# Kernel optimization log

Hardware: AMD Instinct MI355X
Metric: run time of the kernel (lower is better)

## Reference

```python
import jax, jax.numpy as jnp
import numpy as np

N_NODES = 60000
N_EDGES = 300000
FACE_DIM = 32
EDGE_DIM = 16
GF = 64   # EGAT node/edge hidden dim
EF = 32   # NNConv output dim
FF = 32   # placeholder point-transformer dim (zeros path)
TOT = GF + EF + FF  # 128
NEG_SLOPE = 0.01    # torch LeakyReLU default inside DGL EGATConv


def _leaky(x):
    return jnp.where(x >= 0, x, NEG_SLOPE * x)


def _edge_softmax(logits, dst, n):
    # softmax over incoming edges of each destination node (DGL edge_softmax)
    m = jax.ops.segment_max(logits, dst, num_segments=n)
    e = jnp.exp(logits - m[dst])
    s = jax.ops.segment_sum(e, dst, num_segments=n)
    return e / s[dst]


def _egat(h, f, src, dst, n, w_ni, w_nj, w_fij, w_node, attn, bias):
    # DGL EGATConv with num_heads=1 (head dim squeezed)
    f_out = _leaky((h @ w_ni)[src] + (h @ w_nj)[dst] + f @ w_fij + bias)  # (E, GF)
    a = _edge_softmax(f_out @ attn, dst, n)                               # (E,)
    msg = (h @ w_node)[src] * a[:, None]                                  # (E, GF)
    h_out = jax.ops.segment_sum(msg, dst, num_segments=n)                 # (N, GF)
    return h_out, f_out


def setup_inputs() -> dict:
    key = jax.random.key(0)
    ks = iter(jax.random.split(key, 40))

    def w(shape, scale=0.1):
        return jax.random.normal(next(ks), shape, dtype=jnp.float32) * scale

    inp = {
        "face_features": jax.random.normal(next(ks), (N_NODES, FACE_DIM), dtype=jnp.float32),
        "edge_features": jax.random.normal(next(ks), (N_EDGES, EDGE_DIM), dtype=jnp.float32),
        "fp_w": w((FACE_DIM, GF)), "fp_b": w((GF,)),
        "ep_w": w((EDGE_DIM, GF)), "ep_b": w((GF,)),
        "nn_w": w((EDGE_DIM, FACE_DIM * EF), 0.05), "nn_b": w((FACE_DIM * EF,), 0.05),
        "nn_bias": w((EF,)),
        "gate_w": w((TOT, 1)), "gate_b": w((1,)),
        "src": jax.random.randint(next(ks), (N_EDGES,), 0, N_NODES),
        "dst": jax.random.randint(next(ks), (N_EDGES,), 0, N_NODES),
    }
    for L in ("e1", "e2"):
        inp[f"{L}_ni"] = w((GF, GF))
        inp[f"{L}_nj"] = w((GF, GF))
        inp[f"{L}_fij"] = w((GF, GF))
        inp[f"{L}_node"] = w((GF, GF))
        inp[f"{L}_attn"] = w((GF,))
        inp[f"{L}_bias"] = w((GF,))
    return inp


def reference(face_features, edge_features, fp_w, fp_b, ep_w, ep_b,
              nn_w, nn_b, nn_bias, gate_w, gate_b,
              e1_ni, e1_nj, e1_fij, e1_node, e1_attn, e1_bias,
              e2_ni, e2_nj, e2_fij, e2_node, e2_attn, e2_bias,
              src, dst):
    n = face_features.shape[0]
    # --- Gf: two stacked EGATConv layers on projected features ---
    h = face_features @ fp_w + fp_b
    f = edge_features @ ep_w + ep_b
    h, f = _egat(h, f, src, dst, n, e1_ni, e1_nj, e1_fij, e1_node, e1_attn, e1_bias)
    h, f = _egat(h, f, src, dst, n, e2_ni, e2_nj, e2_fij, e2_node, e2_attn, e2_bias)
    Gf = h
    # --- Ef: NNConv (edge-conditioned conv, mean aggregation) ---
    W_e = (edge_features @ nn_w + nn_b).reshape(-1, FACE_DIM, EF)      # (E, 32, 32)
    m = jnp.einsum('ei,eio->eo', face_features[src], W_e)              # (E, EF)
    s = jax.ops.segment_sum(m, dst, num_segments=n)
    cnt = jax.ops.segment_sum(jnp.ones((m.shape[0],), m.dtype), dst, num_segments=n)
    Ef_feat = s / jnp.maximum(cnt, 1.0)[:, None] + nn_bias             # (N, EF)
    # --- Ff: zeros (face_point_features=None path) ---
    Ff_feat = jnp.zeros((n, FF), dtype=Gf.dtype)
    node_features = jnp.concatenate([Gf, Ef_feat, Ff_feat], axis=-1)   # (N, 128)
    # --- GlobalAttentionPooling (single graph) ---
    gate = jax.nn.softmax(node_features @ gate_w + gate_b, axis=0)     # (N, 1)
    graph_feat = jnp.sum(gate * node_features, axis=0, keepdims=True)  # (1, 128)
    return node_features, graph_feat
```

## Files before the change

kernel.cpp:

```cpp
#include <hip/hip_runtime.h>

#define NN 60000
#define NE 300000
#define PB 768
typedef unsigned short ush;
typedef __attribute__((ext_vector_type(8))) short bf16x8;
typedef __attribute__((ext_vector_type(4))) float f32x4;

static inline int cdiv(int a, int b) { return (a + b - 1) / b; }

__device__ inline unsigned ord_enc(float x) {
  unsigned u = __float_as_uint(x);
  return (u & 0x80000000u) ? ~u : (u | 0x80000000u);
}
__device__ inline float ord_dec(unsigned u) {
  return __uint_as_float((u & 0x80000000u) ? (u & 0x7fffffffu) : ~u);
}
__device__ inline float bf2f(unsigned u16) { return __uint_as_float(u16 << 16); }
__device__ inline ush f2bf(float x) {
  unsigned u = __float_as_uint(x);
  return (ush)((u + 0x7FFFu + ((u >> 16) & 1u)) >> 16);
}
__device__ inline unsigned pack2(float lo, float hi) {
  return ((unsigned)f2bf(hi) << 16) | (unsigned)f2bf(lo);
}

__global__ void deg_kernel(const int* __restrict__ key, int* __restrict__ deg) {
  int e = blockIdx.x * blockDim.x + threadIdx.x;
  if (e < NE) atomicAdd(deg + key[e], 1);
}

__global__ void scan1_kernel(const int* __restrict__ deg, int* __restrict__ rowptr,
                             int* __restrict__ partial) {
  __shared__ int s[256];
  int i = blockIdx.x * 256 + threadIdx.x;
  int v = (i < NN) ? deg[i] : 0;
  s[threadIdx.x] = v;
  __syncthreads();
  for (int off = 1; off < 256; off <<= 1) {
    int t = (threadIdx.x >= off) ? s[threadIdx.x - off] : 0;
    __syncthreads();
    s[threadIdx.x] += t;
    __syncthreads();
  }
  if (i < NN) rowptr[i] = s[threadIdx.x] - v;
  if (threadIdx.x == 255) partial[blockIdx.x] = s[255];
}

__global__ void scan2_kernel(int* __restrict__ partial, int nb) {
  __shared__ int s[256];
  int v = (threadIdx.x < nb) ? partial[threadIdx.x] : 0;
  s[threadIdx.x] = v;
  __syncthreads();
  for (int off = 1; off < 256; off <<= 1) {
    int t = (threadIdx.x >= off) ? s[threadIdx.x - off] : 0;
    __syncthreads();
    s[threadIdx.x] += t;
    __syncthreads();
  }
  if (threadIdx.x < nb) partial[threadIdx.x] = s[threadIdx.x] - v;
}

__global__ void scan3_kernel(int* __restrict__ rowptr, const int* __restrict__ partial,
                             int* __restrict__ cursor) {
  int i = blockIdx.x * 256 + threadIdx.x;
  if (i < NN) {
    int r = rowptr[i] + partial[blockIdx.x];
    rowptr[i] = r;
    cursor[i] = r;
  }
}

__global__ void scatter_dst_kernel(const int* __restrict__ src, const int* __restrict__ dst,
                                   const float* __restrict__ ef, int* __restrict__ cursor,
                                   int* __restrict__ src_s, int* __restrict__ dst_s,
                                   float* __restrict__ ef_s) {
  int e = blockIdx.x * blockDim.x + threadIdx.x;
  if (e >= NE) return;
  int d = dst[e];
  int j = atomicAdd(cursor + d, 1);
  src_s[j] = src[e];
  dst_s[j] = d;
  const float4* ep = (const float4*)(ef + (size_t)e * 16);
  float4 a = ep[0], b = ep[1], c = ep[2], dd = ep[3];
  float4* op = (float4*)(ef_s + (size_t)j * 16);
  op[0] = a; op[1] = b; op[2] = c; op[3] = dd;
}

__global__ void fold_kernel(const float* __restrict__ fp_w, const float* __restrict__ fp_b,
                            const float* __restrict__ ep_w, const float* __restrict__ ep_b,
                            const float* __restrict__ fij, const float* __restrict__ ebias,
                            const float* __restrict__ ni, const float* __restrict__ nj,
                            const float* __restrict__ node, float* __restrict__ fold) {
  int t = blockIdx.x * blockDim.x + threadIdx.x;
  if (t >= 7424) return;
  int o = t & 63;
  const float* A;
  const float* B;
  float init = 0.f;
  if (t < 1024)      { A = ep_w + (size_t)(t >> 6) * 64; B = fij + o; }
  else if (t < 1088) { A = ep_b; B = fij + o; init = ebias[o]; }
  else if (t < 3136) { A = fp_w + (size_t)((t - 1088) >> 6) * 64; B = ni + o; }
  else if (t < 5184) { A = fp_w + (size_t)((t - 3136) >> 6) * 64; B = nj + o; }
  else if (t < 7232) { A = fp_w + (size_t)((t - 5184) >> 6) * 64; B = node + o; }
  else if (t < 7296) { A = fp_b; B = ni + o; }
  else if (t < 7360) { A = fp_b; B = nj + o; }
  else               { A = fp_b; B = node + o; }
  float a = init;
  for (int i = 0; i < 64; ++i) a = fmaf(A[i], B[(size_t)i * 64], a);
  fold[t] = a;
}

__global__ void nnwt_frag_kernel(const float* __restrict__ nn_w, const float* __restrict__ nn_b,
                                 ush* __restrict__ Wfrag) {
  int t = blockIdx.x * blockDim.x + threadIdx.x;
  if (t >= 17408) return;
  int i = t & 7, lane = (t >> 3) & 63, ct = (t >> 9) & 1, kk = t >> 10;
  int k = kk * 32 + (lane >> 4) * 8 + i;
  int o = ct * 16 + (lane & 15);
  float v = (k < 512) ? nn_w[(size_t)(k >> 5) * 1024 + (k & 31) * 32 + o]
                      : nn_b[(k - 512) * 32 + o];
  Wfrag[t] = f2bf(v);
}

__global__ void fij_frag_kernel(const float* __restrict__ fij, ush* __restrict__ Wfrag2) {
  int t = blockIdx.x * blockDim.x + threadIdx.x;
  if (t >= 4096) return;
  int i = t & 7, lane = (t >> 3) & 63, ct = (t >> 9) & 3, kk = t >> 11;
  int k = kk * 32 + (lane >> 4) * 8 + i;
  int o = ct * 16 + (lane & 15);
  Wfrag2[t] = f2bf(fij[(size_t)k * 64 + o]);
}

__global__ void hproj_frag_kernel(const float* __restrict__ ni, const float* __restrict__ nj,
                                  const float* __restrict__ node, ush* __restrict__ WfragH) {
  int t = blockIdx.x * blockDim.x + threadIdx.x;
  if (t >= 12288) return;
  int i = t & 7, lane = (t >> 3) & 63, ct = (t >> 9) & 3, kk = (t >> 11) & 1, m = t >> 12;
  int k = kk * 32 + (lane >> 4) * 8 + i;
  int o = ct * 16 + (lane & 15);
  const float* W = (m == 0) ? ni : (m == 1) ? nj : node;
  WfragH[t] = f2bf(W[(size_t)k * 64 + o]);
}

template <int K, bool BIAS>
__global__ __launch_bounds__(256, 2) void gemm3_kernel(
    const float* __restrict__ A, const float* __restrict__ W0, const float* __restrict__ W1,
    const float* __restrict__ W2, const float* __restrict__ b0, const float* __restrict__ b1,
    const float* __restrict__ b2, ush* __restrict__ o0, ush* __restrict__ o1,
    ush* __restrict__ o2, int rows) {
  __shared__ float sA[128][K + 1];
  __shared__ float sW[K][64];
  const float* W = blockIdx.y == 0 ? W0 : blockIdx.y == 1 ? W1 : W2;
  const float* bb = blockIdx.y == 0 ? b0 : blockIdx.y == 1 ? b1 : b2;
  ush* out = blockIdx.y == 0 ? o0 : blockIdx.y == 1 ? o1 : o2;
  int t = threadIdx.x;
  int r0 = blockIdx.x * 128;
  for (int i = t; i < K * 16; i += 256) ((float4*)sW)[i] = ((const float4*)W)[i];
  for (int i = t; i < 128 * (K / 4); i += 256) {
    int rr = i / (K / 4), cc = i % (K / 4);
    float4 v = (r0 + rr < rows) ? ((const float4*)(A + (size_t)(r0 + rr) * K))[cc]
                                : make_float4(0.f, 0.f, 0.f, 0.f);
    sA[rr][cc * 4 + 0] = v.x;
    sA[rr][cc * 4 + 1] = v.y;
    sA[rr][cc * 4 + 2] = v.z;
    sA[rr][cc * 4 + 3] = v.w;
  }
  __syncthreads();
  int rg = t >> 3, cg = t & 7;
  float acc[4][8];
#pragma unroll
  for (int i = 0; i < 4; ++i)
#pragma unroll
    for (int j = 0; j < 8; ++j) acc[i][j] = 0.f;
#pragma unroll 8
  for (int k = 0; k < K; ++k) {
    float a0 = sA[rg * 4 + 0][k], a1 = sA[rg * 4 + 1][k];
    float a2 = sA[rg * 4 + 2][k], a3 = sA[rg * 4 + 3][k];
    float4 wA = *(const float4*)&sW[k][cg * 8];
    float4 wB = *(const float4*)&sW[k][cg * 8 + 4];
#pragma unroll
    for (int i = 0; i < 4; ++i) {
      float a = i == 0 ? a0 : i == 1 ? a1 : i == 2 ? a2 : a3;
      acc[i][0] = fmaf(a, wA.x, acc[i][0]); acc[i][1] = fmaf(a, wA.y, acc[i][1]);
      acc[i][2] = fmaf(a, wA.z, acc[i][2]); acc[i][3] = fmaf(a, wA.w, acc[i][3]);
      acc[i][4] = fmaf(a, wB.x, acc[i][4]); acc[i][5] = fmaf(a, wB.y, acc[i][5]);
      acc[i][6] = fmaf(a, wB.z, acc[i][6]); acc[i][7] = fmaf(a, wB.w, acc[i][7]);
    }
  }
  float bv[8];
#pragma unroll
  for (int j = 0; j < 8; ++j) bv[j] = BIAS ? bb[cg * 8 + j] : 0.f;
#pragma unroll
  for (int i = 0; i < 4; ++i) {
    int r = r0 + rg * 4 + i;
    if (r < rows) {
      uint4 pv;
      pv.x = pack2(acc[i][0] + bv[0], acc[i][1] + bv[1]);
      pv.y = pack2(acc[i][2] + bv[2], acc[i][3] + bv[3]);
      pv.z = pack2(acc[i][4] + bv[4], acc[i][5] + bv[5]);
      pv.w = pack2(acc[i][6] + bv[6], acc[i][7] + bv[7]);
      *(uint4*)(out + (size_t)r * 64 + cg * 8) = pv;
    }
  }
}

template <int K, bool STORE>
__global__ __launch_bounds__(256, 2) void gemm_fout_kernel(
    const float* __restrict__ A, const float* __restrict__ W, const float* __restrict__ bias,
    const ush* __restrict__ hs, const ush* __restrict__ hd, const int* __restrict__ src_s,
    const int* __restrict__ dst_s, const float* __restrict__ attn, ush* __restrict__ fstore,
    float* __restrict__ logit) {
  __shared__ float sA[128][K + 1];
  __shared__ float sW[K][64];
  int t = threadIdx.x;
  int r0 = blockIdx.x * 128;
  for (int i = t; i < K * 16; i += 256) ((float4*)sW)[i] = ((const float4*)W)[i];
  for (int i = t; i < 128 * (K / 4); i += 256) {
    int rr = i / (K / 4), cc = i % (K / 4);
    float4 v = (r0 + rr < NE) ? ((const float4*)(A + (size_t)(r0 + rr) * K))[cc]
                              : make_float4(0.f, 0.f, 0.f, 0.f);
    sA[rr][cc * 4 + 0] = v.x;
    sA[rr][cc * 4 + 1] = v.y;
    sA[rr][cc * 4 + 2] = v.z;
    sA[rr][cc * 4 + 3] = v.w;
  }
  __syncthreads();
  int rg = t >> 3, cg = t & 7;
  float acc[4][8];
#pragma unroll
  for (int i = 0; i < 4; ++i)
#pragma unroll
    for (int j = 0; j < 8; ++j) acc[i][j] = 0.f;
#pragma unroll 8
  for (int k = 0; k < K; ++k) {
    float a0 = sA[rg * 4 + 0][k], a1 = sA[rg * 4 + 1][k];
    float a2 = sA[rg * 4 + 2][k], a3 = sA[rg * 4 + 3][k];
    float4 wA = *(const float4*)&sW[k][cg * 8];
    float4 wB = *(const float4*)&sW[k][cg * 8 + 4];
#pragma unroll
    for (int i = 0; i < 4; ++i) {
      float a = i == 0 ? a0 : i == 1 ? a1 : i == 2 ? a2 : a3;
      acc[i][0] = fmaf(a, wA.x, acc[i][0]); acc[i][1] = fmaf(a, wA.y, acc[i][1]);
      acc[i][2] = fmaf(a, wA.z, acc[i][2]); acc[i][3] = fmaf(a, wA.w, acc[i][3]);
      acc[i][4] = fmaf(a, wB.x, acc[i][4]); acc[i][5] = fmaf(a, wB.y, acc[i][5]);
      acc[i][6] = fmaf(a, wB.z, acc[i][6]); acc[i][7] = fmaf(a, wB.w, acc[i][7]);
    }
  }
  float bv[8], av[8];
#pragma unroll
  for (int j = 0; j < 8; ++j) {
    bv[j] = bias[cg * 8 + j];
    av[j] = attn[cg * 8 + j];
  }
#pragma unroll
  for (int i = 0; i < 4; ++i) {
    int r = r0 + rg * 4 + i;
    if (r < NE) {
      int s = src_s[r], d = dst_s[r];
      uint4 hv = *(const uint4*)(hs + (size_t)s * 64 + cg * 8);
      uint4 dv = *(const uint4*)(hd + (size_t)d * 64 + cg * 8);
      float fo[8];
      fo[0] = acc[i][0] + bf2f(hv.x & 0xffff) + bf2f(dv.x & 0xffff) + bv[0];
      fo[1] = acc[i][1] + bf2f(hv.x >> 16)    + bf2f(dv.x >> 16)    + bv[1];
      fo[2] = acc[i][2] + bf2f(hv.y & 0xffff) + bf2f(dv.y & 0xffff) + bv[2];
      fo[3] = acc[i][3] + bf2f(hv.y >> 16)    + bf2f(dv.y >> 16)    + bv[3];
      fo[4] = acc[i][4] + bf2f(hv.z & 0xffff) + bf2f(dv.z & 0xffff) + bv[4];
      fo[5] = acc[i][5] + bf2f(hv.z >> 16)    + bf2f(dv.z >> 16)    + bv[5];
      fo[6] = acc[i][6] + bf2f(hv.w & 0xffff) + bf2f(dv.w & 0xffff) + bv[6];
      fo[7] = acc[i][7] + bf2f(hv.w >> 16)    + bf2f(dv.w >> 16)    + bv[7];
      float p = 0.f;
#pragma unroll
      for (int j = 0; j < 8; ++j) {
        fo[j] = fo[j] >= 0.f ? fo[j] : 0.01f * fo[j];
        p = fmaf(fo[j], av[j], p);
      }
      if (STORE) {
        uint4 pv;
        pv.x = pack2(fo[0], fo[1]);
        pv.y = pack2(fo[2], fo[3]);
        pv.z = pack2(fo[4], fo[5]);
        pv.w = pack2(fo[6], fo[7]);
        *(uint4*)(fstore + (size_t)r * 64 + cg * 8) = pv;
      }
      p += __shfl_xor(p, 1, 64);
      p += __shfl_xor(p, 2, 64);
      p += __shfl_xor(p, 4, 64);
      if (cg == 0) logit[r] = p;
    }
  }
}

__global__ __launch_bounds__(256, 4) void mfma_hproj_kernel(
    const ush* __restrict__ h1bf, const ush* __restrict__ WfragH, ush* __restrict__ hs,
    ush* __restrict__ hd, ush* __restrict__ hn) {
  int wave = (blockIdx.x * blockDim.x + threadIdx.x) >> 6;
  int lane = threadIdx.x & 63;
  int m0 = wave * 16;
  if (m0 >= NN) return;
  int arow = lane & 15;
  int aoff = (lane >> 4) * 8;
  const ush* ap = h1bf + (size_t)(m0 + arow) * 64 + aoff;
  bf16x8 a0 = *(const bf16x8*)(ap);
  bf16x8 a1 = *(const bf16x8*)(ap + 32);
  const ush* wp = WfragH + lane * 8;
  int ccol = lane & 15;
  int crow = (lane >> 4) * 4;
#pragma unroll
  for (int m = 0; m < 3; ++m) {
    f32x4 acc0 = {0.f, 0.f, 0.f, 0.f};
    f32x4 acc1 = {0.f, 0.f, 0.f, 0.f};
    f32x4 acc2 = {0.f, 0.f, 0.f, 0.f};
    f32x4 acc3 = {0.f, 0.f, 0.f, 0.f};
    const ush* wm = wp + (size_t)m * 8 * 512;
    bf16x8 b0 = *(const bf16x8*)(wm + 0 * 512);
    bf16x8 b1 = *(const bf16x8*)(wm + 1 * 512);
    bf16x8 b2 = *(const bf16x8*)(wm + 2 * 512);
    bf16x8 b3 = *(const bf16x8*)(wm + 3 * 512);
    acc0 = __builtin_amdgcn_mfma_f32_16x16x32_bf16(a0, b0, acc0, 0, 0, 0);
    acc1 = __builtin_amdgcn_mfma_f32_16x16x32_bf16(a0, b1, acc1, 0, 0, 0);
    acc2 = __builtin_amdgcn_mfma_f32_16x16x32_bf16(a0, b2, acc2, 0, 0, 0);
    acc3 = __builtin_amdgcn_mfma_f32_16x16x32_bf16(a0, b3, acc3, 0, 0, 0);
    b0 = *(const bf16x8*)(wm + 4 * 512);
    b1 = *(const bf16x8*)(wm + 5 * 512);
    b2 = *(const bf16x8*)(wm + 6 * 512);
    b3 = *(const bf16x8*)(wm + 7 * 512);
    acc0 = __builtin_amdgcn_mfma_f32_16x16x32_bf16(a1, b0, acc0, 0, 0, 0);
    acc1 = __builtin_amdgcn_mfma_f32_16x16x32_bf16(a1, b1, acc1, 0, 0, 0);
    acc2 = __builtin_amdgcn_mfma_f32_16x16x32_bf16(a1, b2, acc2, 0, 0, 0);
    acc3 = __builtin_amdgcn_mfma_f32_16x16x32_bf16(a1, b3, acc3, 0, 0, 0);
    ush* outm = (m == 0) ? hs : (m == 1) ? hd : hn;
#pragma unroll
    for (int j = 0; j < 4; ++j) {
      ush* op = outm + (size_t)(m0 + crow + j) * 64;
      op[ccol] = f2bf(acc0[j]);
      op[16 + ccol] = f2bf(acc1[j]);
      op[32 + ccol] = f2bf(acc2[j]);
      op[48 + ccol] = f2bf(acc3[j]);
    }
  }
}

__global__ __launch_bounds__(256, 4) void mfma_fout_kernel(
    const ush* __restrict__ f116, const ush* __restrict__ Wfrag2, const float* __restrict__ bias,
    const ush* __restrict__ hs, const ush* __restrict__ hd, const int* __restrict__ src_s,
    const int* __restrict__ dst_s, const float* __restrict__ attn, float* __restrict__ logit) {
  int wave = (blockIdx.x * blockDim.x + threadIdx.x) >> 6;
  int lane = threadIdx.x & 63;
  int m0 = wave * 16;
  if (m0 >= NE) return;
  int arow = lane & 15;
  int aoff = (lane >> 4) * 8;
  const ush* ap = f116 + (size_t)(m0 + arow) * 64 + aoff;
  const ush* wp = Wfrag2 + lane * 8;
  f32x4 acc0 = {0.f, 0.f, 0.f, 0.f};
  f32x4 acc1 = {0.f, 0.f, 0.f, 0.f};
  f32x4 acc2 = {0.f, 0.f, 0.f, 0.f};
  f32x4 acc3 = {0.f, 0.f, 0.f, 0.f};
#pragma unroll
  for (int kk = 0; kk < 2; ++kk) {
    bf16x8 a = *(const bf16x8*)(ap + kk * 32);
    bf16x8 b0 = *(const bf16x8*)(wp + (size_t)(kk * 4 + 0) * 512);
    bf16x8 b1 = *(const bf16x8*)(wp + (size_t)(kk * 4 + 1) * 512);
    bf16x8 b2 = *(const bf16x8*)(wp + (size_t)(kk * 4 + 2) * 512);
    bf16x8 b3 = *(const bf16x8*)(wp + (size_t)(kk * 4 + 3) * 512);
    acc0 = __builtin_amdgcn_mfma_f32_16x16x32_bf16(a, b0, acc0, 0, 0, 0);
    acc1 = __builtin_amdgcn_mfma_f32_16x16x32_bf16(a, b1, acc1, 0, 0, 0);
    acc2 = __builtin_amdgcn_mfma_f32_16x16x32_bf16(a, b2, acc2, 0, 0, 0);
    acc3 = __builtin_amdgcn_mfma_f32_16x16x32_bf16(a, b3, acc3, 0, 0, 0);
  }
  int ccol = lane & 15;
  int crow = (lane >> 4) * 4;
  float av0 = attn[ccol], av1 = attn[16 + ccol], av2 = attn[32 + ccol], av3 = attn[48 + ccol];
  float bv0 = bias[ccol], bv1 = bias[16 + ccol], bv2 = bias[32 + ccol], bv3 = bias[48 + ccol];
#pragma unroll
  for (int j = 0; j < 4; ++j) {
    int r = m0 + crow + j;
    int s = src_s[r], d = dst_s[r];
    const ush* hsp = hs + (size_t)s * 64;
    const ush* hdp = hd + (size_t)d * 64;
    float f0 = acc0[j] + bf2f(hsp[ccol]) + bf2f(hdp[ccol]) + bv0;
    float f1 = acc1[j] + bf2f(hsp[16 + ccol]) + bf2f(hdp[16 + ccol]) + bv1;
    float f2 = acc2[j] + bf2f(hsp[32 + ccol]) + bf2f(hdp[32 + ccol]) + bv2;
    float f3 = acc3[j] + bf2f(hsp[48 + ccol]) + bf2f(hdp[48 + ccol]) + bv3;
    f0 = f0 >= 0.f ? f0 : 0.01f * f0;
    f1 = f1 >= 0.f ? f1 : 0.01f * f1;
    f2 = f2 >= 0.f ? f2 : 0.01f * f2;
    f3 = f3 >= 0.f ? f3 : 0.01f * f3;
    float p = fmaf(f0, av0, fmaf(f1, av1, fmaf(f2, av2, f3 * av3)));
    p += __shfl_xor(p, 1, 64);
    p += __shfl_xor(p, 2, 64);
    p += __shfl_xor(p, 4, 64);
    p += __shfl_xor(p, 8, 64);
    if (ccol == 0) logit[r] = p;
  }
}

template <bool BF16OUT>
__global__ __launch_bounds__(256, 4) void agg_gather_kernel(
    const ush* __restrict__ hn, const float* __restrict__ logit, const int* __restrict__ rowptr,
    const int* __restrict__ deg, const int* __restrict__ src_s, void* __restrict__ hnew) {
  int wave = (blockIdx.x * blockDim.x + threadIdx.x) >> 6;
  int lane = threadIdx.x & 63;
  if (wave >= NN) return;
  int n = wave, d = deg[n], r0 = rowptr[n];
  if (d == 0) {
    if (BF16OUT) ((ush*)hnew)[(size_t)n * 64 + lane] = 0;
    else ((float*)hnew)[(size_t)n * 64 + lane] = 0.f;
    return;
  }
  float sum = 0.f, acc0 = 0.f, acc1 = 0.f, acc2 = 0.f, acc3 = 0.f;
  int j = 0;
  for (; j + 3 < d; j += 4) {
    int jj = r0 + j;
    int s0 = src_s[jj + 0], s1 = src_s[jj + 1], s2 = src_s[jj + 2], s3 = src_s[jj + 3];
    float l0 = logit[jj + 0], l1 = logit[jj + 1], l2 = logit[jj + 2], l3 = logit[jj + 3];
    ush h0 = hn[(size_t)s0 * 64 + lane];
    ush h1 = hn[(size_t)s1 * 64 + lane];
    ush h2 = hn[(size_t)s2 * 64 + lane];
    ush h3 = hn[(size_t)s3 * 64 + lane];
    float w0 = __expf(l0), w1 = __expf(l1);
    float w2 = __expf(l2), w3 = __expf(l3);
    sum += (w0 + w1) + (w2 + w3);
    acc0 = fmaf(w0, bf2f(h0), acc0);
    acc1 = fmaf(w1, bf2f(h1), acc1);
    acc2 = fmaf(w2, bf2f(h2), acc2);
    acc3 = fmaf(w3, bf2f(h3), acc3);
  }
  for (; j < d; ++j) {
    int jj = r0 + j;
    float w = __expf(logit[jj]);
    sum += w;
    acc0 = fmaf(w, bf2f(hn[(size_t)src_s[jj] * 64 + lane]), acc0);
  }
  float r = ((acc0 + acc1) + (acc2 + acc3)) / sum;
  if (BF16OUT) ((ush*)hnew)[(size_t)n * 64 + lane] = f2bf(r);
  else ((float*)hnew)[(size_t)n * 64 + lane] = r;
}

__global__ __launch_bounds__(256, 4) void nnconv_G_kernel(
    const float* __restrict__ face, const float* __restrict__ ef_s,
    const int* __restrict__ rowptr, const int* __restrict__ deg, const int* __restrict__ src_s,
    ush* __restrict__ G) {
  int wave = (blockIdx.x * blockDim.x + threadIdx.x) >> 6;
  int lane = threadIdx.x & 63;
  if (wave >= NN) return;
  int n = wave, d = deg[n], r0 = rowptr[n];
  int k4 = lane >> 2, ib = lane & 3;
  float g[8], fs[8];
#pragma unroll
  for (int u = 0; u < 8; ++u) { g[u] = 0.f; fs[u] = 0.f; }
  int j = 0;
  for (; j + 1 < d; j += 2) {
    int jj = r0 + j;
    int s0 = src_s[jj], s1 = src_s[jj + 1];
    float ev0 = ef_s[(size_t)jj * 16 + k4];
    float ev1 = ef_s[(size_t)(jj + 1) * 16 + k4];
    const float4* fp0 = (const float4*)(face + (size_t)s0 * 32 + ib * 8);
    const float4* fp1 = (const float4*)(face + (size_t)s1 * 32 + ib * 8);
    float4 fa0 = fp0[0], fb0 = fp0[1];
    float4 fa1 = fp1[0], fb1 = fp1[1];
    g[0] = fmaf(ev0, fa0.x, g[0]); g[1] = fmaf(ev0, fa0.y, g[1]);
    g[2] = fmaf(ev0, fa0.z, g[2]); g[3] = fmaf(ev0, fa0.w, g[3]);
    g[4] = fmaf(ev0, fb0.x, g[4]); g[5] = fmaf(ev0, fb0.y, g[5]);
    g[6] = fmaf(ev0, fb0.z, g[6]); g[7] = fmaf(ev0, fb0.w, g[7]);
    g[0] = fmaf(ev1, fa1.x, g[0]); g[1] = fmaf(ev1, fa1.y, g[1]);
    g[2] = fmaf(ev1, fa1.z, g[2]); g[3] = fmaf(ev1, fa1.w, g[3]);
    g[4] = fmaf(ev1, fb1.x, g[4]); g[5] = fmaf(ev1, fb1.y, g[5]);
    g[6] = fmaf(ev1, fb1.z, g[6]); g[7] = fmaf(ev1, fb1.w, g[7]);
    if (k4 == 0) {
      fs[0] += fa0.x + fa1.x; fs[1] += fa0.y + fa1.y;
      fs[2] += fa0.z + fa1.z; fs[3] += fa0.w + fa1.w;
      fs[4] += fb0.x + fb1.x; fs[5] += fb0.y + fb1.y;
      fs[6] += fb0.z + fb1.z; fs[7] += fb0.w + fb1.w;
    }
  }
  if (j < d) {
    int jj = r0 + j;
    int s0 = src_s[jj];
    float ev0 = ef_s[(size_t)jj * 16 + k4];
    const float4* fp0 = (const float4*)(face + (size_t)s0 * 32 + ib * 8);
    float4 fa0 = fp0[0], fb0 = fp0[1];
    g[0] = fmaf(ev0, fa0.x, g[0]); g[1] = fmaf(ev0, fa0.y, g[1]);
    g[2] = fmaf(ev0, fa0.z, g[2]); g[3] = fmaf(ev0, fa0.w, g[3]);
    g[4] = fmaf(ev0, fb0.x, g[4]); g[5] = fmaf(ev0, fb0.y, g[5]);
    g[6] = fmaf(ev0, fb0.z, g[6]); g[7] = fmaf(ev0, fb0.w, g[7]);
    if (k4 == 0) {
      fs[0] += fa0.x; fs[1] += fa0.y; fs[2] += fa0.z; fs[3] += fa0.w;
      fs[4] += fb0.x; fs[5] += fb0.y; fs[6] += fb0.z; fs[7] += fb0.w;
    }
  }
  uint4 pv;
  pv.x = pack2(g[0], g[1]); pv.y = pack2(g[2], g[3]);
  pv.z = pack2(g[4], g[5]); pv.w = pack2(g[6], g[7]);
  *(uint4*)(G + (size_t)n * 544 + lane * 8) = pv;
  if (k4 == 0) {
    uint4 fv;
    fv.x = pack2(fs[0], fs[1]); fv.y = pack2(fs[2], fs[3]);
    fv.z = pack2(fs[4], fs[5]); fv.w = pack2(fs[6], fs[7]);
    *(uint4*)(G + (size_t)n * 544 + 512 + ib * 8) = fv;
  }
}

__global__ __launch_bounds__(256, 4) void gemm_G_mfma_kernel(const ush* __restrict__ G,
                                                             const ush* __restrict__ Wfrag,
                                                             float* __restrict__ sArr,
                                                             int rows) {
  int wave = (blockIdx.x * blockDim.x + threadIdx.x) >> 6;
  int lane = threadIdx.x & 63;
  int m0 = wave * 16;
  if (m0 >= rows) return;
  int arow = lane & 15;
  int aoff = (lane >> 4) * 8;
  const ush* gp = G + (size_t)(m0 + arow) * 544 + aoff;
  const ush* wp = Wfrag + lane * 8;
  f32x4 acc0 = {0.f, 0.f, 0.f, 0.f};
  f32x4 acc1 = {0.f, 0.f, 0.f, 0.f};
#pragma unroll 4
  for (int kk = 0; kk < 17; ++kk) {
    bf16x8 a = *(const bf16x8*)(gp + kk * 32);
    bf16x8 b0 = *(const bf16x8*)(wp + (size_t)(kk * 2 + 0) * 512);
    bf16x8 b1 = *(const bf16x8*)(wp + (size_t)(kk * 2 + 1) * 512);
    acc0 = __builtin_amdgcn_mfma_f32_16x16x32_bf16(a, b0, acc0, 0, 0, 0);
    acc1 = __builtin_amdgcn_mfma_f32_16x16x32_bf16(a, b1, acc1, 0, 0, 0);
  }
  int ccol = lane & 15;
  int crow = (lane >> 4) * 4;
#pragma unroll
  for (int j = 0; j < 4; ++j) {
    int r = m0 + crow + j;
    sArr[(size_t)r * 32 + ccol] = acc0[j];
    sArr[(size_t)r * 32 + 16 + ccol] = acc1[j];
  }
}

__global__ void combine_gate_kernel(const float* __restrict__ hfin, const float* __restrict__ sArr,
                                    const int* __restrict__ deg, const float* __restrict__ nn_bias,
                                    const float* __restrict__ gate_w, const float* __restrict__ gate_b,
                                    float* __restrict__ out, float* __restrict__ g) {
  int wave = (blockIdx.x * blockDim.x + threadIdx.x) >> 6;
  int lane = threadIdx.x & 63;
  if (wave >= NN) return;
  int n = wave;
  float v0 = hfin[(size_t)n * 64 + lane];
  int c1 = lane + 64;
  float v1 = (c1 < 96)
                 ? sArr[(size_t)n * 32 + (c1 - 64)] / fmaxf((float)deg[n], 1.0f) + nn_bias[c1 - 64]
                 : 0.f;
  out[(size_t)n * 128 + lane] = v0;
  out[(size_t)n * 128 + c1] = v1;
  float p = v0 * gate_w[lane] + ((c1 < 96) ? v1 * gate_w[c1] : 0.f);
#pragma unroll
  for (int off = 32; off; off >>= 1) p += __shfl_xor(p, off, 64);
  if (lane == 0) g[n] = p + gate_b[0];
}

__global__ void gate_max_kernel(const float* __restrict__ g, unsigned* __restrict__ gmax) {
  int tid = blockIdx.x * blockDim.x + threadIdx.x;
  int stride = gridDim.x * blockDim.x;
  float v = -3.0e38f;
  for (int n = tid; n < NN; n += stride) v = fmaxf(v, g[n]);
#pragma unroll
  for (int off = 32; off; off >>= 1) v = fmaxf(v, __shfl_xor(v, off, 64));
  __shared__ float sm[4];
  int lane = threadIdx.x & 63, wid = threadIdx.x >> 6;
  if (lane == 0) sm[wid] = v;
  __syncthreads();
  if (threadIdx.x == 0) {
    float m = fmaxf(fmaxf(sm[0], sm[1]), fmaxf(sm[2], sm[3]));
    atomicMax(gmax, ord_enc(m));
  }
}

__global__ __launch_bounds__(256, 4) void pool_exp_kernel(
    const float* __restrict__ nf, const float* __restrict__ g, const unsigned* __restrict__ gmax,
    float* __restrict__ pacc, float* __restrict__ wsb) {
  int o = threadIdx.x & 127;
  int half = threadIdx.x >> 7;
  int ri = blockIdx.x * 2 + half;
  float m = ord_dec(*gmax);
  float acc0 = 0.f, acc1 = 0.f, ws = 0.f;
  int n = ri;
  const int STR = PB * 2;
  for (; n + STR < NN; n += STR * 2) {
    float w0 = __expf(g[n] - m);
    float w1 = __expf(g[n + STR] - m);
    float v0 = nf[(size_t)n * 128 + o];
    float v1 = nf[(size_t)(n + STR) * 128 + o];
    ws += w0 + w1;
    acc0 = fmaf(w0, v0, acc0);
    acc1 = fmaf(w1, v1, acc1);
  }
  if (n < NN) {
    float w = __expf(g[n] - m);
    ws += w;
    acc0 = fmaf(w, nf[(size_t)n * 128 + o], acc0);
  }
  pacc[(size_t)ri * 128 + o] = acc0 + acc1;
  if (o == 0) wsb[ri] = ws;
}

__global__ void pool_reduce_kernel(const float* __restrict__ pacc, const float* __restrict__ wsb,
                                   float* __restrict__ gacc, float* __restrict__ gsum) {
  int b = blockIdx.x;
  int t = threadIdx.x;
  float v = 0.f;
  if (b < 128) {
    for (int ri = t; ri < PB * 2; ri += 256) v += pacc[(size_t)ri * 128 + b];
  } else {
    for (int ri = t; ri < PB * 2; ri += 256) v += wsb[ri];
  }
#pragma unroll
  for (int off = 32; off; off >>= 1) v += __shfl_xor(v, off, 64);
  __shared__ float sm[4];
  int lane = t & 63, wid = t >> 6;
  if (lane == 0) sm[wid] = v;
  __syncthreads();
  if (t == 0) {
    float s = (sm[0] + sm[1]) + (sm[2] + sm[3]);
    if (b < 128) gacc[b] = s;
    else gsum[0] = s;
  }
}

__global__ void finalize_kernel(const float* __restrict__ gacc, const float* __restrict__ gsum,
                                float* __restrict__ out) {
  int o = threadIdx.x;
  if (o < 128) out[(size_t)NN * 128 + o] = gacc[o] / gsum[0];
}

extern "C" void kernel_launch(void* const* d_in, const int* in_sizes, int n_in,
                              void* d_out, int out_size, void* d_ws, size_t ws_size,
                              hipStream_t stream) {
  const float* face    = (const float*)d_in[0];
  const float* ef      = (const float*)d_in[1];
  const float* fp_w    = (const float*)d_in[2];
  const float* fp_b    = (const float*)d_in[3];
  const float* ep_w    = (const float*)d_in[4];
  const float* ep_b    = (const float*)d_in[5];
  const float* nn_w    = (const float*)d_in[6];
  const float* nn_b    = (const float*)d_in[7];
  const float* nn_bias = (const float*)d_in[8];
  const float* gate_w  = (const float*)d_in[9];
  const float* gate_b  = (const float*)d_in[10];
  const int*   src     = (const int*)d_in[11];
  const int*   dst     = (const int*)d_in[12];
  const float* e1_attn = (const float*)d_in[17];
  const float* e2_ni   = (const float*)d_in[19];
  const float* e2_nj   = (const float*)d_in[20];
  const float* e2_fij  = (const float*)d_in[21];
  const float* e2_attn = (const float*)d_in[23];
  const float* e2_bias = (const float*)d_in[24];
  float* out = (float*)d_out;

  char* p = (char*)d_ws;
  auto alloc = [&](size_t nfloats) {
    float* r = (float*)p;
    p += ((nfloats * 4 + 255) / 256) * 256;
    return r;
  };
  float* h0 = alloc((size_t)NN * 64);
  ush* h1bf = (ush*)alloc((size_t)NN * 32);
  char* bigreg = p;
  ush* hs16 = (ush*)alloc((size_t)NN * 32);
  ush* hd16 = (ush*)alloc((size_t)NN * 32);
  ush* hn16 = (ush*)alloc((size_t)NN * 32);
  ush* f116 = (ush*)alloc((size_t)NE * 32);
  float* logit = alloc(NE);
  {
    size_t used = (size_t)(p - bigreg);
    size_t need = (size_t)NN * 544 * 2;
    if (used < need) p += ((need - used + 255) / 256) * 256;
  }
  ush* G = (ush*)bigreg;
  float* sArr  = alloc((size_t)NN * 32);
  float* g     = alloc(NN);
  float* gacc  = alloc(128);
  float* gsum  = alloc(1);
  unsigned* gmax = (unsigned*)alloc(1);
  float* fold  = alloc(7424);
  ush* Wfrag   = (ush*)alloc(17408 / 2);
  ush* Wfrag2  = (ush*)alloc(4096 / 2);
  ush* WfragH  = (ush*)alloc(12288 / 2);
  float* pacc  = alloc((size_t)PB * 2 * 128);
  float* wsb   = alloc(PB * 2);
  int* deg    = (int*)alloc(NN);
  int* rowptr = (int*)alloc(NN);
  int* cursor = (int*)alloc(NN);
  int* partial = (int*)alloc(256);
  int* src_s  = (int*)alloc(NE);
  int* dst_s  = (int*)alloc(NE);
  float* ef_s = alloc((size_t)NE * 16);

  const float* Wf1  = fold;
  const float* b1f  = fold + 1024;
  const float* Wni1 = fold + 1088;
  const float* Wnj1 = fold + 3136;
  const float* Wno1 = fold + 5184;
  const float* bni1 = fold + 7232;
  const float* bnj1 = fold + 7296;
  const float* bno1 = fold + 7360;

  const int B = 256;
  const int NGB = cdiv(NN, 128);
  const int EGB = cdiv(NE, 128);
  const int NB256 = cdiv(NN, 256);

  hipMemsetAsync(deg, 0, NN * 4, stream);
  deg_kernel<<<cdiv(NE, B), B, 0, stream>>>(dst, deg);
  scan1_kernel<<<NB256, 256, 0, stream>>>(deg, rowptr, partial);
  scan2_kernel<<<1, 256, 0, stream>>>(partial, NB256);
  scan3_kernel<<<NB256, 256, 0, stream>>>(rowptr, partial, cursor);
  scatter_dst_kernel<<<cdiv(NE, B), B, 0, stream>>>(src, dst, ef, cursor, src_s, dst_s, ef_s);

  fold_kernel<<<29, B, 0, stream>>>(fp_w, fp_b, ep_w, ep_b,
                                    (const float*)d_in[15], (const float*)d_in[18],
                                    (const float*)d_in[13], (const float*)d_in[14],
                                    (const float*)d_in[16], fold);
  nnwt_frag_kernel<<<68, B, 0, stream>>>(nn_w, nn_b, Wfrag);
  fij_frag_kernel<<<16, B, 0, stream>>>(e2_fij, Wfrag2);
  hproj_frag_kernel<<<48, B, 0, stream>>>(e2_ni, e2_nj, (const float*)d_in[22], WfragH);

  gemm3_kernel<32, true><<<dim3(NGB, 3), B, 0, stream>>>(face, Wni1, Wnj1, Wno1, bni1, bnj1,
                                                         bno1, hs16, hd16, hn16, NN);
  gemm_fout_kernel<16, true><<<EGB, B, 0, stream>>>(ef_s, Wf1, b1f, hs16, hd16, src_s,
                                                    dst_s, e1_attn, f116, logit);
  agg_gather_kernel<true><<<cdiv(NN * 64, B), B, 0, stream>>>(hn16, logit, rowptr, deg,
                                                              src_s, h1bf);

  mfma_hproj_kernel<<<cdiv(NN * 4, B), B, 0, stream>>>(h1bf, WfragH, hs16, hd16, hn16);
  mfma_fout_kernel<<<cdiv(NE * 4, B), B, 0, stream>>>(f116, Wfrag2, e2_bias, hs16, hd16,
                                                      src_s, dst_s, e2_attn, logit);
  agg_gather_kernel<false><<<cdiv(NN * 64, B), B, 0, stream>>>(hn16, logit, rowptr, deg,
                                                               src_s, h0);

  nnconv_G_kernel<<<cdiv(NN * 64, B), B, 0, stream>>>(face, ef_s, rowptr, deg, src_s, G);
  gemm_G_mfma_kernel<<<cdiv(NN * 4, B), B, 0, stream>>>(G, Wfrag, sArr, NN);

  hipMemsetAsync(gmax, 0, 4, stream);
  combine_gate_kernel<<<cdiv(NN * 64, B), B, 0, stream>>>(h0, sArr, deg, nn_bias, gate_w,
                                                          gate_b, out, g);
  gate_max_kernel<<<128, B, 0, stream>>>(g, gmax);
  pool_exp_kernel<<<PB, B, 0, stream>>>(out, g, gmax, pacc, wsb);
  pool_reduce_kernel<<<129, B, 0, stream>>>(pacc, wsb, gacc, gsum);
  finalize_kernel<<<1, 128, 0, stream>>>(gacc, gsum, out);
}
```

Measured before the change: 265.4 us.

## Replace layer-1 FP32 SIMT GEMMs with bf16 MFMA kernels

The first EGAT layer's node projection and edge f_out GEMMs are switched from LDS-tiled FP32 FMA kernels to one-wave-per-16-rows bf16 MFMA kernels, matching the layer-2 path. Face features get a bf16 copy from a new conversion kernel. Edge features get a bf16 copy, zero-padded to K=32, written in the scatter kernel, and the folded weights are repacked into MFMA fragment layout. This removes the scalar FMA loops and LDS staging. In exchange it adds an extra launch, extra padded bf16 edge traffic, narrow 2-byte scattered output stores, and bf16 rounding of the layer-1 inputs.

```diff
diff --git a/kernel.cpp b/kernel.cpp
--- a/kernel.cpp
+++ b/kernel.cpp
@@ -74,7 +74,7 @@
 __global__ void scatter_dst_kernel(const int* __restrict__ src, const int* __restrict__ dst,
                                    const float* __restrict__ ef, int* __restrict__ cursor,
                                    int* __restrict__ src_s, int* __restrict__ dst_s,
-                                   float* __restrict__ ef_s) {
+                                   float* __restrict__ ef_s, ush* __restrict__ ef16) {
   int e = blockIdx.x * blockDim.x + threadIdx.x;
   if (e >= NE) return;
   int d = dst[e];
@@ -85,6 +85,22 @@
   float4 a = ep[0], b = ep[1], c = ep[2], dd = ep[3];
   float4* op = (float4*)(ef_s + (size_t)j * 16);
   op[0] = a; op[1] = b; op[2] = c; op[3] = dd;
+  uint4* bp = (uint4*)(ef16 + (size_t)j * 32);
+  uint4 p0, p1;
+  p0.x = pack2(a.x, a.y); p0.y = pack2(a.z, a.w);
+  p0.z = pack2(b.x, b.y); p0.w = pack2(b.z, b.w);
+  p1.x = pack2(c.x, c.y); p1.y = pack2(c.z, c.w);
+  p1.z = pack2(dd.x, dd.y); p1.w = pack2(dd.z, dd.w);
+  bp[0] = p0; bp[1] = p1;
+  bp[2] = make_uint4(0, 0, 0, 0);
+  bp[3] = make_uint4(0, 0, 0, 0);
+}
+
+__global__ void face16_kernel(const float* __restrict__ face, ush* __restrict__ face16) {
+  int t = blockIdx.x * blockDim.x + threadIdx.x;
+  if (t >= NN * 8) return;
+  const float4 v = ((const float4*)face)[t];
+  ((uint2*)face16)[t] = make_uint2(pack2(v.x, v.y), pack2(v.z, v.w));
 }
 
 __global__ void fold_kernel(const float* __restrict__ fp_w, const float* __restrict__ fp_b,
@@ -111,6 +127,24 @@
   fold[t] = a;
 }
 
+__global__ void fold1_frag_kernel(const float* __restrict__ fold, ush* __restrict__ Wf1frag,
+                                  ush* __restrict__ WfragH1) {
+  int t = blockIdx.x * blockDim.x + threadIdx.x;
+  if (t >= 2048 + 6144) return;
+  if (t < 2048) {
+    int i = t & 7, lane = (t >> 3) & 63, ct = t >> 9;
+    int k = (lane >> 4) * 8 + i;
+    int o = ct * 16 + (lane & 15);
+    Wf1frag[t] = (k < 16) ? f2bf(fold[(size_t)k * 64 + o]) : 0;
+  } else {
+    int idx = t - 2048;
+    int i = idx & 7, lane = (idx >> 3) & 63, ct = (idx >> 9) & 3, m = idx >> 11;
+    int k = (lane >> 4) * 8 + i;
+    int o = ct * 16 + (lane & 15);
+    WfragH1[idx] = f2bf(fold[1088 + (size_t)m * 2048 + (size_t)k * 64 + o]);
+  }
+}
+
 __global__ void nnwt_frag_kernel(const float* __restrict__ nn_w, const float* __restrict__ nn_b,
                                  ush* __restrict__ Wfrag) {
   int t = blockIdx.x * blockDim.x + threadIdx.x;
@@ -143,151 +177,105 @@
   WfragH[t] = f2bf(W[(size_t)k * 64 + o]);
 }
 
-template <int K, bool BIAS>
-__global__ __launch_bounds__(256, 2) void gemm3_kernel(
-    const float* __restrict__ A, const float* __restrict__ W0, const float* __restrict__ W1,
-    const float* __restrict__ W2, const float* __restrict__ b0, const float* __restrict__ b1,
-    const float* __restrict__ b2, ush* __restrict__ o0, ush* __restrict__ o1,
-    ush* __restrict__ o2, int rows) {
-  __shared__ float sA[128][K + 1];
-  __shared__ float sW[K][64];
-  const float* W = blockIdx.y == 0 ? W0 : blockIdx.y == 1 ? W1 : W2;
-  const float* bb = blockIdx.y == 0 ? b0 : blockIdx.y == 1 ? b1 : b2;
-  ush* out = blockIdx.y == 0 ? o0 : blockIdx.y == 1 ? o1 : o2;
-  int t = threadIdx.x;
-  int r0 = blockIdx.x * 128;
-  for (int i = t; i < K * 16; i += 256) ((float4*)sW)[i] = ((const float4*)W)[i];
-  for (int i = t; i < 128 * (K / 4); i += 256) {
-    int rr = i / (K / 4), cc = i % (K / 4);
-    float4 v = (r0 + rr < rows) ? ((const float4*)(A + (size_t)(r0 + rr) * K))[cc]
-                                : make_float4(0.f, 0.f, 0.f, 0.f);
-    sA[rr][cc * 4 + 0] = v.x;
-    sA[rr][cc * 4 + 1] = v.y;
-    sA[rr][cc * 4 + 2] = v.z;
-    sA[rr][cc * 4 + 3] = v.w;
-  }
-  __syncthreads();
-  int rg = t >> 3, cg = t & 7;
-  float acc[4][8];
-#pragma unroll
-  for (int i = 0; i < 4; ++i)
-#pragma unroll
-    for (int j = 0; j < 8; ++j) acc[i][j] = 0.f;
-#pragma unroll 8
-  for (int k = 0; k < K; ++k) {
-    float a0 = sA[rg * 4 + 0][k], a1 = sA[rg * 4 + 1][k];
-    float a2 = sA[rg * 4 + 2][k], a3 = sA[rg * 4 + 3][k];
-    float4 wA = *(const float4*)&sW[k][cg * 8];
-    float4 wB = *(const float4*)&sW[k][cg * 8 + 4];
-#pragma unroll
-    for (int i = 0; i < 4; ++i) {
-      float a = i == 0 ? a0 : i == 1 ? a1 : i == 2 ? a2 : a3;
-      acc[i][0] = fmaf(a, wA.x, acc[i][0]); acc[i][1] = fmaf(a, wA.y, acc[i][1]);
-      acc[i][2] = fmaf(a, wA.z, acc[i][2]); acc[i][3] = fmaf(a, wA.w, acc[i][3]);
-      acc[i][4] = fmaf(a, wB.x, acc[i][4]); acc[i][5] = fmaf(a, wB.y, acc[i][5]);
-      acc[i][6] = fmaf(a, wB.z, acc[i][6]); acc[i][7] = fmaf(a, wB.w, acc[i][7]);
+__global__ __launch_bounds__(256, 4) void mfma_hproj1_kernel(
+    const ush* __restrict__ face16, const ush* __restrict__ WfragH1,
+    const float* __restrict__ fold, ush* __restrict__ hs, ush* __restrict__ hd,
+    ush* __restrict__ hn) {
+  int wave = (blockIdx.x * blockDim.x + threadIdx.x) >> 6;
+  int lane = threadIdx.x & 63;
+  int m0 = wave * 16;
+  if (m0 >= NN) return;
+  int arow = lane & 15;
+  int aoff = (lane >> 4) * 8;
+  bf16x8 a = *(const bf16x8*)(face16 + (size_t)(m0 + arow) * 32 + aoff);
+  int ccol = lane & 15;
+  int crow = (lane >> 4) * 4;
+#pragma unroll
+  for (int m = 0; m < 3; ++m) {
+    const ush* wm = WfragH1 + (size_t)m * 2048 + lane * 8;
+    bf16x8 b0 = *(const bf16x8*)(wm + 0 * 512);
+    bf16x8 b1 = *(const bf16x8*)(wm + 1 * 512);
+    bf16x8 b2 = *(const bf16x8*)(wm + 2 * 512);
+    bf16x8 b3 = *(const bf16x8*)(wm + 3 * 512);
+    f32x4 acc0 = {0.f, 0.f, 0.f, 0.f};
+    f32x4 acc1 = {0.f, 0.f, 0.f, 0.f};
+    f32x4 acc2 = {0.f, 0.f, 0.f, 0.f};
+    f32x4 acc3 = {0.f, 0.f, 0.f, 0.f};
+    acc0 = __builtin_amdgcn_mfma_f32_16x16x32_bf16(a, b0, acc0, 0, 0, 0);
+    acc1 = __builtin_amdgcn_mfma_f32_16x16x32_bf16(a, b1, acc1, 0, 0, 0);
+    acc2 = __builtin_amdgcn_mfma_f32_16x16x32_bf16(a, b2, acc2, 0, 0, 0);
+    acc3 = __builtin_amdgcn_mfma_f32_16x16x32_bf16(a, b3, acc3, 0, 0, 0);
+    float bv0 = fold[7232 + m * 64 + ccol];
+    float bv1 = fold[7232 + m * 64 + 16 + ccol];
+    float bv2 = fold[7232 + m * 64 + 32 + ccol];
+    float bv3 = fold[7232 + m * 64 + 48 + ccol];
+    ush* outm = (m == 0) ? hs : (m == 1) ? hd : hn;
+#pragma unroll
+    for (int j = 0; j < 4; ++j) {
+      ush* op = outm + (size_t)(m0 + crow + j) * 64;
+      op[ccol] = f2bf(acc0[j] + bv0);
+      op[16 + ccol] = f2bf(acc1[j] + bv1);
+      op[32 + ccol] = f2bf(acc2[j] + bv2);
+      op[48 + ccol] = f2bf(acc3[j] + bv3);
     }
   }
-  float bv[8];
-#pragma unroll
-  for (int j = 0; j < 8; ++j) bv[j] = BIAS ? bb[cg * 8 + j] : 0.f;
-#pragma unroll
-  for (int i = 0; i < 4; ++i) {
-    int r = r0 + rg * 4 + i;
-    if (r < rows) {
-      uint4 pv;
-      pv.x = pack2(acc[i][0] + bv[0], acc[i][1] + bv[1]);
-      pv.y = pack2(acc[i][2] + bv[2], acc[i][3] + bv[3]);
-      pv.z = pack2(acc[i][4] + bv[4], acc[i][5] + bv[5]);
-      pv.w = pack2(acc[i][6] + bv[6], acc[i][7] + bv[7]);
-      *(uint4*)(out + (size_t)r * 64 + cg * 8) = pv;
-    }
-  }
-}
-
-template <int K, bool STORE>
-__global__ __launch_bounds__(256, 2) void gemm_fout_kernel(
-    const float* __restrict__ A, const float* __restrict__ W, const float* __restrict__ bias,
+}
+
+__global__ __launch_bounds__(256, 4) void mfma_fout1_kernel(
+    const ush* __restrict__ ef16, const ush* __restrict__ Wf1frag, const float* __restrict__ fold,
     const ush* __restrict__ hs, const ush* __restrict__ hd, const int* __restrict__ src_s,
-    const int* __restrict__ dst_s, const float* __restrict__ attn, ush* __restrict__ fstore,
+    const int* __restrict__ dst_s, const float* __restrict__ attn, ush* __restrict__ f116,
     float* __restrict__ logit) {
-  __shared__ float sA[128][K + 1];
-  __shared__ float sW[K][64];
-  int t = threadIdx.x;
-  int r0 = blockIdx.x * 128;
-  for (int i = t; i < K * 16; i += 256) ((float4*)sW)[i] = ((const float4*)W)[i];
-  for (int i = t; i < 128 * (K / 4); i += 256) {
-    int rr = i / (K / 4), cc = i % (K / 4);
-    float4 v = (r0 + rr < NE) ? ((const float4*)(A + (size_t)(r0 + rr) * K))[cc]
-                              : make_float4(0.f, 0.f, 0.f, 0.f);
-    sA[rr][cc * 4 + 0] = v.x;
-    sA[rr][cc * 4 + 1] = v.y;
-    sA[rr][cc * 4 + 2] = v.z;
-    sA[rr][cc * 4 + 3] = v.w;
-  }
-  __syncthreads();
-  int rg = t >> 3, cg = t & 7;
-  float acc[4][8];
-#pragma unroll
-  for (int i = 0; i < 4; ++i)
-#pragma unroll
-    for (int j = 0; j < 8; ++j) acc[i][j] = 0.f;
-#pragma unroll 8
-  for (int k = 0; k < K; ++k) {
-    float a0 = sA[rg * 4 + 0][k], a1 = sA[rg * 4 + 1][k];
-    float a2 = sA[rg * 4 + 2][k], a3 = sA[rg * 4 + 3][k];
-    float4 wA = *(const float4*)&sW[k][cg * 8];
-    float4 wB = *(const float4*)&sW[k][cg * 8 + 4];
-#pragma unroll
-    for (int i = 0; i < 4; ++i) {
-      float a = i == 0 ? a0 : i == 1 ? a1 : i == 2 ? a2 : a3;
-      acc[i][0] = fmaf(a, wA.x, acc[i][0]); acc[i][1] = fmaf(a, wA.y, acc[i][1]);
-      acc[i][2] = fmaf(a, wA.z, acc[i][2]); acc[i][3] = fmaf(a, wA.w, acc[i][3]);
-      acc[i][4] = fmaf(a, wB.x, acc[i][4]); acc[i][5] = fmaf(a, wB.y, acc[i][5]);
-      acc[i][6] = fmaf(a, wB.z, acc[i][6]); acc[i][7] = fmaf(a, wB.w, acc[i][7]);
-    }
-  }
-  float bv[8], av[8];
-#pragma unroll
-  for (int j = 0; j < 8; ++j) {
-    bv[j] = bias[cg * 8 + j];
-    av[j] = attn[cg * 8 + j];
-  }
-#pragma unroll
-  for (int i = 0; i < 4; ++i) {
-    int r = r0 + rg * 4 + i;
-    if (r < NE) {
-      int s = src_s[r], d = dst_s[r];
-      uint4 hv = *(const uint4*)(hs + (size_t)s * 64 + cg * 8);
-      uint4 dv = *(const uint4*)(hd + (size_t)d * 64 + cg * 8);
-      float fo[8];
-      fo[0] = acc[i][0] + bf2f(hv.x & 0xffff) + bf2f(dv.x & 0xffff) + bv[0];
-      fo[1] = acc[i][1] + bf2f(hv.x >> 16)    + bf2f(dv.x >> 16)    + bv[1];
-      fo[2] = acc[i][2] + bf2f(hv.y & 0xffff) + bf2f(dv.y & 0xffff) + bv[2];
-      fo[3] = acc[i][3] + bf2f(hv.y >> 16)    + bf2f(dv.y >> 16)    + bv[3];
-      fo[4] = acc[i][4] + bf2f(hv.z & 0xffff) + bf2f(dv.z & 0xffff) + bv[4];
-      fo[5] = acc[i][5] + bf2f(hv.z >> 16)    + bf2f(dv.z >> 16)    + bv[5];
-      fo[6] = acc[i][6] + bf2f(hv.w & 0xffff) + bf2f(dv.w & 0xffff) + bv[6];
-      fo[7] = acc[i][7] + bf2f(hv.w >> 16)    + bf2f(dv.w >> 16)    + bv[7];
-      float p = 0.f;
-#pragma unroll
-      for (int j = 0; j < 8; ++j) {
-        fo[j] = fo[j] >= 0.f ? fo[j] : 0.01f * fo[j];
-        p = fmaf(fo[j], av[j], p);
-      }
-      if (STORE) {
-        uint4 pv;
-        pv.x = pack2(fo[0], fo[1]);
-        pv.y = pack2(fo[2], fo[3]);
-        pv.z = pack2(fo[4], fo[5]);
-        pv.w = pack2(fo[6], fo[7]);
-        *(uint4*)(fstore + (size_t)r * 64 + cg * 8) = pv;
-      }
-      p += __shfl_xor(p, 1, 64);
-      p += __shfl_xor(p, 2, 64);
-      p += __shfl_xor(p, 4, 64);
-      if (cg == 0) logit[r] = p;
-    }
+  int wave = (blockIdx.x * blockDim.x + threadIdx.x) >> 6;
+  int lane = threadIdx.x & 63;
+  int m0 = wave * 16;
+  if (m0 >= NE) return;
+  int arow = lane & 15;
+  int aoff = (lane >> 4) * 8;
+  bf16x8 a = *(const bf16x8*)(ef16 + (size_t)(m0 + arow) * 32 + aoff);
+  const ush* wp = Wf1frag + lane * 8;
+  bf16x8 b0 = *(const bf16x8*)(wp + 0 * 512);
+  bf16x8 b1 = *(const bf16x8*)(wp + 1 * 512);
+  bf16x8 b2 = *(const bf16x8*)(wp + 2 * 512);
+  bf16x8 b3 = *(const bf16x8*)(wp + 3 * 512);
+  f32x4 acc0 = {0.f, 0.f, 0.f, 0.f};
+  f32x4 acc1 = {0.f, 0.f, 0.f, 0.f};
+  f32x4 acc2 = {0.f, 0.f, 0.f, 0.f};
+  f32x4 acc3 = {0.f, 0.f, 0.f, 0.f};
+  acc0 = __builtin_amdgcn_mfma_f32_16x16x32_bf16(a, b0, acc0, 0, 0, 0);
+  acc1 = __builtin_amdgcn_mfma_f32_16x16x32_bf16(a, b1, acc1, 0, 0, 0);
+  acc2 = __builtin_amdgcn_mfma_f32_16x16x32_bf16(a, b2, acc2, 0, 0, 0);
+  acc3 = __builtin_amdgcn_mfma_f32_16x16x32_bf16(a, b3, acc3, 0, 0, 0);
+  int ccol = lane & 15;
+  int crow = (lane >> 4) * 4;
+  float av0 = attn[ccol], av1 = attn[16 + ccol], av2 = attn[32 + ccol], av3 = attn[48 + ccol];
+  float bv0 = fold[1024 + ccol], bv1 = fold[1024 + 16 + ccol];
+  float bv2 = fold[1024 + 32 + ccol], bv3 = fold[1024 + 48 + ccol];
+#pragma unroll
+  for (int j = 0; j < 4; ++j) {
+    int r = m0 + crow + j;
+    int s = src_s[r], d = dst_s[r];
+    const ush* hsp = hs + (size_t)s * 64;
+    const ush* hdp = hd + (size_t)d * 64;
+    float f0 = acc0[j] + bf2f(hsp[ccol]) + bf2f(hdp[ccol]) + bv0;
+    float f1 = acc1[j] + bf2f(hsp[16 + ccol]) + bf2f(hdp[16 + ccol]) + bv1;
+    float f2 = acc2[j] + bf2f(hsp[32 + ccol]) + bf2f(hdp[32 + ccol]) + bv2;
+    float f3 = acc3[j] + bf2f(hsp[48 + ccol]) + bf2f(hdp[48 + ccol]) + bv3;
+    f0 = f0 >= 0.f ? f0 : 0.01f * f0;
+    f1 = f1 >= 0.f ? f1 : 0.01f * f1;
+    f2 = f2 >= 0.f ? f2 : 0.01f * f2;
+    f3 = f3 >= 0.f ? f3 : 0.01f * f3;
+    ush* fp = f116 + (size_t)r * 64;
+    fp[ccol] = f2bf(f0);
+    fp[16 + ccol] = f2bf(f1);
+    fp[32 + ccol] = f2bf(f2);
+    fp[48 + ccol] = f2bf(f3);
+    float p = fmaf(f0, av0, fmaf(f1, av1, fmaf(f2, av2, f3 * av3)));
+    p += __shfl_xor(p, 1, 64);
+    p += __shfl_xor(p, 2, 64);
+    p += __shfl_xor(p, 4, 64);
+    p += __shfl_xor(p, 8, 64);
+    if (ccol == 0) logit[r] = p;
   }
 }
 
@@ -682,6 +670,10 @@
   ush* Wfrag   = (ush*)alloc(17408 / 2);
   ush* Wfrag2  = (ush*)alloc(4096 / 2);
   ush* WfragH  = (ush*)alloc(12288 / 2);
+  ush* Wf1frag = (ush*)alloc(2048 / 2);
+  ush* WfragH1 = (ush*)alloc(6144 / 2);
+  ush* face16  = (ush*)alloc((size_t)NN * 16);
+  ush* ef16    = (ush*)alloc((size_t)NE * 16);
   float* pacc  = alloc((size_t)PB * 2 * 128);
   float* wsb   = alloc(PB * 2);
   int* deg    = (int*)alloc(NN);
@@ -692,18 +684,7 @@
   int* dst_s  = (int*)alloc(NE);
   float* ef_s = alloc((size_t)NE * 16);
 
-  const float* Wf1  = fold;
-  const float* b1f  = fold + 1024;
-  const float* Wni1 = fold + 1088;
-  const float* Wnj1 = fold + 3136;
-  const float* Wno1 = fold + 5184;
-  const float* bni1 = fold + 7232;
-  const float* bnj1 = fold + 7296;
-  const float* bno1 = fold + 7360;
-
   const int B = 256;
-  const int NGB = cdiv(NN, 128);
-  const int EGB = cdiv(NE, 128);
   const int NB256 = cdiv(NN, 256);
 
   hipMemsetAsync(deg, 0, NN * 4, stream);
@@ -711,20 +692,22 @@
   scan1_kernel<<<NB256, 256, 0, stream>>>(deg, rowptr, partial);
   scan2_kernel<<<1, 256, 0, stream>>>(partial, NB256);
   scan3_kernel<<<NB256, 256, 0, stream>>>(rowptr, partial, cursor);
-  scatter_dst_kernel<<<cdiv(NE, B), B, 0, stream>>>(src, dst, ef, cursor, src_s, dst_s, ef_s);
+  scatter_dst_kernel<<<cdiv(NE, B), B, 0, stream>>>(src, dst, ef, cursor, src_s, dst_s,
+                                                    ef_s, ef16);
 
   fold_kernel<<<29, B, 0, stream>>>(fp_w, fp_b, ep_w, ep_b,
                                     (const float*)d_in[15], (const float*)d_in[18],
                                     (const float*)d_in[13], (const float*)d_in[14],
                                     (const float*)d_in[16], fold);
+  fold1_frag_kernel<<<32, B, 0, stream>>>(fold, Wf1frag, WfragH1);
   nnwt_frag_kernel<<<68, B, 0, stream>>>(nn_w, nn_b, Wfrag);
   fij_frag_kernel<<<16, B, 0, stream>>>(e2_fij, Wfrag2);
   hproj_frag_kernel<<<48, B, 0, stream>>>(e2_ni, e2_nj, (const float*)d_in[22], WfragH);
-
-  gemm3_kernel<32, true><<<dim3(NGB, 3), B, 0, stream>>>(face, Wni1, Wnj1, Wno1, bni1, bnj1,
-                                                         bno1, hs16, hd16, hn16, NN);
-  gemm_fout_kernel<16, true><<<EGB, B, 0, stream>>>(ef_s, Wf1, b1f, hs16, hd16, src_s,
-                                                    dst_s, e1_attn, f116, logit);
+  face16_kernel<<<cdiv(NN * 8, B), B, 0, stream>>>(face, face16);
+
+  mfma_hproj1_kernel<<<cdiv(NN * 4, B), B, 0, stream>>>(face16, WfragH1, fold, hs16, hd16, hn16);
+  mfma_fout1_kernel<<<cdiv(NE * 4, B), B, 0, stream>>>(ef16, Wf1frag, fold, hs16, hd16,
+                                                       src_s, dst_s, e1_attn, f116, logit);
   agg_gather_kernel<true><<<cdiv(NN * 64, B), B, 0, stream>>>(hn16, logit, rowptr, deg,
                                                               src_s, h1bf);
 
```

After: 259.1 us. 1.02x faster.
